# Kernel tuning notes

Hardware: AMD Instinct MI355X
Metric: run time of the kernel (lower is better)

## Reference

```python
import jax, jax.numpy as jnp
import numpy as np

N = 100000
E = 1600000
H = 4
C = 128
F_IN = 182
D = H * C  # 512
NEG_SLOPE = 0.2
LN_EPS = 1e-5


def _p(key, shape, scale=0.05):
    return jax.random.normal(key, shape, dtype=jnp.float32) * scale


def setup_inputs() -> dict:
    key = jax.random.key(0)
    ks = jax.random.split(key, 20)
    x = jax.random.normal(ks[0], (N, F_IN), dtype=jnp.float32)
    edge_index = jax.random.randint(ks[1], (2, E), 0, N, dtype=jnp.int64)
    inp = {
        "x": x,
        "edge_index": edge_index,
        # GAT layer 1
        "W1": _p(ks[2], (F_IN, D)),
        "a_src1": _p(ks[3], (H, C)),
        "a_dst1": _p(ks[4], (H, C)),
        "b1": _p(ks[5], (D,)),
        "g1": jnp.ones((D,), jnp.float32),
        "be1": jnp.zeros((D,), jnp.float32),
        # GAT layer 2
        "W2": _p(ks[6], (D, D)),
        "a_src2": _p(ks[7], (H, C)),
        "a_dst2": _p(ks[8], (H, C)),
        "b2": _p(ks[9], (D,)),
        "g2": jnp.ones((D,), jnp.float32),
        "be2": jnp.zeros((D,), jnp.float32),
        # classifier MLP
        "Wc1": _p(ks[10], (D, D)),
        "bc1": jnp.zeros((D,), jnp.float32),
        "Wc2": _p(ks[11], (D, 2)),
        "bc2": jnp.zeros((2,), jnp.float32),
    }
    return inp


def _gat_conv(x, src, dst, W, a_src, a_dst, b):
    # x: [N, Fin] -> h: [N, H, C]
    h = (x @ W).reshape(N, H, C)
    # per-node attention contributions: [N, H]
    s_src = jnp.sum(h * a_src, axis=-1)
    s_dst = jnp.sum(h * a_dst, axis=-1)
    # per-edge raw score: [E+N, H]
    e = jax.nn.leaky_relu(s_src[src] + s_dst[dst], NEG_SLOPE)
    # segment softmax over incoming edges of each dst node
    emax = jax.ops.segment_max(e, dst, num_segments=N)
    p = jnp.exp(e - emax[dst])
    denom = jax.ops.segment_sum(p, dst, num_segments=N)
    alpha = p / denom[dst]  # [E+N, H]
    # weighted aggregation of source features: [N, H, C]
    out = jax.ops.segment_sum(alpha[:, :, None] * h[src], dst, num_segments=N)
    return out.reshape(N, D) + b


def _layer_norm(x, g, b):
    mu = jnp.mean(x, axis=-1, keepdims=True)
    var = jnp.mean(jnp.square(x - mu), axis=-1, keepdims=True)
    return (x - mu) * jax.lax.rsqrt(var + LN_EPS) * g + b


def reference(x, edge_index, W1, a_src1, a_dst1, b1, g1, be1,
              W2, a_src2, a_dst2, b2, g2, be2, Wc1, bc1, Wc2, bc2):
    # add self-loops (PyG GATConv default)
    loops = jnp.arange(N, dtype=edge_index.dtype)
    src = jnp.concatenate([edge_index[0], loops])
    dst = jnp.concatenate([edge_index[1], loops])

    h1 = _gat_conv(x, src, dst, W1, a_src1, a_dst1, b1)
    h1 = jax.nn.elu(_layer_norm(h1, g1, be1))
    h2 = _gat_conv(h1, src, dst, W2, a_src2, a_dst2, b2)
    h2 = jax.nn.elu(_layer_norm(h2, g2, be2))
    # classifier (dropout is identity in eval)
    z = jax.nn.relu(h2 @ Wc1 + bc1)
    return z @ Wc2 + bc2
```

## Files before the change

### kernel.cpp

```cpp
#include <hip/hip_runtime.h>
#include <math.h>

static constexpr int N_NODES = 100000;
static constexpr int N_EDGES = 1600000;
static constexpr int E_TOT   = N_NODES + N_EDGES;
static constexpr int D   = 512;
static constexpr int FIN = 182;
static constexpr int K1P = 192;
static constexpr int M_PAD = 100096;
static constexpr float NEG_SLOPE = 0.2f;
static constexpr float LN_EPS = 1e-5f;

typedef __attribute__((ext_vector_type(8))) short short8;
typedef __attribute__((ext_vector_type(4))) float floatx4;

__device__ __forceinline__ unsigned short f2bf(float f) {
  unsigned int x = __builtin_bit_cast(unsigned int, f);
  x += 0x7fffu + ((x >> 16) & 1u);
  return (unsigned short)(x >> 16);
}
__device__ __forceinline__ void unpack2(unsigned int w, float& lo, float& hi) {
  lo = __builtin_bit_cast(float, w << 16);
  hi = __builtin_bit_cast(float, w & 0xffff0000u);
}

typedef __attribute__((address_space(1))) const void gv_t;
typedef __attribute__((address_space(3))) void lv_t;
__device__ __forceinline__ void gll16(const void* g, void* l) {
  __builtin_amdgcn_global_load_lds((gv_t*)g, (lv_t*)l, 16, 0, 0);
}

__global__ __launch_bounds__(256) void k_init(int* __restrict__ deg,
                                              int* __restrict__ counter,
                                              int* __restrict__ flag) {
  int i = blockIdx.x * 256 + threadIdx.x;
  if (i < N_NODES) deg[i] = 0;
  if (i == 0) { *counter = 0; *flag = 0; }
}

__global__ __launch_bounds__(256) void k_detect(const int* __restrict__ ei,
                                                int* __restrict__ flag) {
  bool nz = false;
#pragma unroll
  for (int r = 0; r < 8; ++r) {
    int i = threadIdx.x + r * 256;
    nz |= (ei[2 * i + 1] != 0);
  }
  __shared__ int sh[4];
  int wv = threadIdx.x >> 6;
  if ((threadIdx.x & 63) == 0) sh[wv] = 0;
  __syncthreads();
  if (__any(nz) && (threadIdx.x & 63) == 0) sh[wv] = 1;
  __syncthreads();
  if (threadIdx.x == 0) *flag = sh[0] | sh[1] | sh[2] | sh[3];
}

__device__ __forceinline__ int edge_src(const int* ei, int f, int i) {
  return f ? ei[i] : ei[2 * i];
}
__device__ __forceinline__ int edge_dst(const int* ei, int f, int i) {
  return f ? ei[N_EDGES + i] : ei[2 * (N_EDGES + i)];
}

__global__ __launch_bounds__(256) void k_count(const int* __restrict__ ei,
                                               const int* __restrict__ flag,
                                               int* __restrict__ deg) {
  int i = blockIdx.x * 256 + threadIdx.x;
  if (i >= E_TOT) return;
  int f = *flag;
  int d = (i < N_EDGES) ? edge_dst(ei, f, i) : (i - N_EDGES);
  atomicAdd(deg + d, 1);
}

__global__ __launch_bounds__(256) void k_alloc(const int* __restrict__ deg,
                                               int* __restrict__ off,
                                               int* __restrict__ pos,
                                               int* __restrict__ counter) {
  int i = blockIdx.x * 256 + threadIdx.x;
  if (i >= N_NODES) return;
  int r = atomicAdd(counter, deg[i]);
  off[i] = r;
  pos[i] = r;
}

__global__ __launch_bounds__(256) void k_fill(const int* __restrict__ ei,
                                              const int* __restrict__ flag,
                                              int* __restrict__ pos,
                                              int* __restrict__ csr_src) {
  int i = blockIdx.x * 256 + threadIdx.x;
  if (i >= E_TOT) return;
  int f = *flag;
  int s, d;
  if (i < N_EDGES) { s = edge_src(ei, f, i); d = edge_dst(ei, f, i); }
  else             { s = d = i - N_EDGES; }
  int slot = atomicAdd(pos + d, 1);
  csr_src[slot] = s;
}

__global__ __launch_bounds__(256) void k_cvt_x(const float* __restrict__ x,
                                               unsigned short* __restrict__ xb) {
  int i = blockIdx.x * 256 + threadIdx.x;
  if (i >= N_NODES * K1P) return;
  int row = i / K1P, col = i - row * K1P;
  float v = (col < FIN) ? x[(size_t)row * FIN + col] : 0.f;
  xb[i] = f2bf(v);
}

__global__ __launch_bounds__(256) void k_cvt_wt(const float* __restrict__ W,
                                                unsigned short* __restrict__ Wt,
                                                int K, int Kpad) {
  int i = blockIdx.x * 256 + threadIdx.x;
  if (i >= 512 * Kpad) return;
  int n = i / Kpad, k = i - n * Kpad;
  Wt[i] = f2bf(k < K ? W[(size_t)k * 512 + n] : 0.f);
}

__global__ __launch_bounds__(256) void k_out_init(const float* __restrict__ bc2,
                                                  float* __restrict__ out) {
  int i = blockIdx.x * 256 + threadIdx.x;
  if (i < N_NODES) {
    float2 v; v.x = bc2[0]; v.y = bc2[1];
    ((float2*)out)[i] = v;
  }
}

__global__ __launch_bounds__(256)
void gemm_mfma(const unsigned short* __restrict__ A,
               const unsigned short* __restrict__ Bt,
               unsigned short* __restrict__ C,
               int lda)
{
  __shared__ unsigned short As[128 * 32];
  __shared__ unsigned short Bs[128 * 32];
  const int t    = threadIdx.x;
  const int w    = t >> 6;
  const int lane = t & 63;
  const int r    = lane & 15;
  const int q    = lane >> 4;
  const int bm   = blockIdx.y * 128;
  const int bn   = blockIdx.x * 128;
  const int wm   = (w >> 1) * 64;
  const int wn   = (w & 1) * 64;

  const int ch0 = (w * 2 + 0) * 64 + lane;
  const int ch1 = (w * 2 + 1) * 64 + lane;
  const unsigned short* gA0 = A + (size_t)(bm + (ch0 >> 2)) * lda + (ch0 & 3) * 8;
  const unsigned short* gA1 = A + (size_t)(bm + (ch1 >> 2)) * lda + (ch1 & 3) * 8;
  const unsigned short* gB0 = Bt + (size_t)(bn + (ch0 >> 2)) * lda + (ch0 & 3) * 8;
  const unsigned short* gB1 = Bt + (size_t)(bn + (ch1 >> 2)) * lda + (ch1 & 3) * 8;
  unsigned short* lA0 = As + (w * 2 + 0) * 512;
  unsigned short* lA1 = As + (w * 2 + 1) * 512;
  unsigned short* lB0 = Bs + (w * 2 + 0) * 512;
  unsigned short* lB1 = Bs + (w * 2 + 1) * 512;

  floatx4 acc[4][4] = {};

  for (int k0 = 0; k0 < lda; k0 += 32) {
    gll16(gA0 + k0, lA0);
    gll16(gA1 + k0, lA1);
    gll16(gB0 + k0, lB0);
    gll16(gB1 + k0, lB1);
    __syncthreads();

    short8 af[4], bfr[4];
#pragma unroll
    for (int im = 0; im < 4; ++im)
      af[im] = *(const short8*)(As + (wm + im * 16 + r) * 32 + q * 8);
#pragma unroll
    for (int in = 0; in < 4; ++in)
      bfr[in] = *(const short8*)(Bs + (wn + in * 16 + r) * 32 + q * 8);
#pragma unroll
    for (int im = 0; im < 4; ++im)
#pragma unroll
      for (int in = 0; in < 4; ++in)
        acc[im][in] = __builtin_amdgcn_mfma_f32_16x16x32_bf16(
            af[im], bfr[in], acc[im][in], 0, 0, 0);
    __syncthreads();
  }

#pragma unroll
  for (int in = 0; in < 4; ++in) {
    const int col = bn + wn + in * 16 + r;
#pragma unroll
    for (int im = 0; im < 4; ++im) {
      const size_t rowbase = (size_t)(bm + wm + im * 16 + q * 4) * 512 + col;
#pragma unroll
      for (int rr = 0; rr < 4; ++rr)
        C[rowbase + (size_t)rr * 512] = f2bf(acc[im][in][rr]);
    }
  }
}

__global__ __launch_bounds__(256)
void gemm_cls(const unsigned short* __restrict__ A,
              const unsigned short* __restrict__ Bt,
              const float* __restrict__ bc1,
              const float* __restrict__ Wc2,
              float* __restrict__ out,
              int lda)
{
  __shared__ unsigned short As[128 * 32];
  __shared__ unsigned short Bs[128 * 32];
  const int t    = threadIdx.x;
  const int w    = t >> 6;
  const int lane = t & 63;
  const int r    = lane & 15;
  const int q    = lane >> 4;
  const int bm   = blockIdx.y * 128;
  const int bn   = blockIdx.x * 128;
  const int wm   = (w >> 1) * 64;
  const int wn   = (w & 1) * 64;

  const int ch0 = (w * 2 + 0) * 64 + lane;
  const int ch1 = (w * 2 + 1) * 64 + lane;
  const unsigned short* gA0 = A + (size_t)(bm + (ch0 >> 2)) * lda + (ch0 & 3) * 8;
  const unsigned short* gA1 = A + (size_t)(bm + (ch1 >> 2)) * lda + (ch1 & 3) * 8;
  const unsigned short* gB0 = Bt + (size_t)(bn + (ch0 >> 2)) * lda + (ch0 & 3) * 8;
  const unsigned short* gB1 = Bt + (size_t)(bn + (ch1 >> 2)) * lda + (ch1 & 3) * 8;
  unsigned short* lA0 = As + (w * 2 + 0) * 512;
  unsigned short* lA1 = As + (w * 2 + 1) * 512;
  unsigned short* lB0 = Bs + (w * 2 + 0) * 512;
  unsigned short* lB1 = Bs + (w * 2 + 1) * 512;

  floatx4 acc[4][4] = {};

  for (int k0 = 0; k0 < lda; k0 += 32) {
    gll16(gA0 + k0, lA0);
    gll16(gA1 + k0, lA1);
    gll16(gB0 + k0, lB0);
    gll16(gB1 + k0, lB1);
    __syncthreads();

    short8 af[4], bfr[4];
#pragma unroll
    for (int im = 0; im < 4; ++im)
      af[im] = *(const short8*)(As + (wm + im * 16 + r) * 32 + q * 8);
#pragma unroll
    for (int in = 0; in < 4; ++in)
      bfr[in] = *(const short8*)(Bs + (wn + in * 16 + r) * 32 + q * 8);
#pragma unroll
    for (int im = 0; im < 4; ++im)
#pragma unroll
      for (int in = 0; in < 4; ++in)
        acc[im][in] = __builtin_amdgcn_mfma_f32_16x16x32_bf16(
            af[im], bfr[in], acc[im][in], 0, 0, 0);
    __syncthreads();
  }

  float p0[16], p1[16];
#pragma unroll
  for (int k = 0; k < 16; ++k) { p0[k] = 0.f; p1[k] = 0.f; }

#pragma unroll
  for (int in = 0; in < 4; ++in) {
    const int col = bn + wn + in * 16 + r;
    const float bv = bc1[col];
    const float w0 = Wc2[col * 2 + 0];
    const float w1 = Wc2[col * 2 + 1];
#pragma unroll
    for (int im = 0; im < 4; ++im)
#pragma unroll
      for (int rr = 0; rr < 4; ++rr) {
        float z = fmaxf(acc[im][in][rr] + bv, 0.f);
        p0[im * 4 + rr] += z * w0;
        p1[im * 4 + rr] += z * w1;
      }
  }
#pragma unroll
  for (int o2 = 1; o2 < 16; o2 <<= 1) {
#pragma unroll
    for (int k = 0; k < 16; ++k) {
      p0[k] += __shfl_xor(p0[k], o2);
      p1[k] += __shfl_xor(p1[k], o2);
    }
  }
  if (r == 0) {
#pragma unroll
    for (int im = 0; im < 4; ++im)
#pragma unroll
      for (int rr = 0; rr < 4; ++rr) {
        int row = bm + wm + im * 16 + q * 4 + rr;
        if (row < N_NODES) {
          atomicAdd(out + (size_t)row * 2,     p0[im * 4 + rr]);
          atomicAdd(out + (size_t)row * 2 + 1, p1[im * 4 + rr]);
        }
      }
  }
}

__global__ __launch_bounds__(256) void k_sdots(const unsigned short* __restrict__ h,
                                               const float* __restrict__ a_src,
                                               const float* __restrict__ a_dst,
                                               float* __restrict__ s_src,
                                               float* __restrict__ s_dst,
                                               unsigned char* __restrict__ h8,
                                               float* __restrict__ scales) {
  int node = blockIdx.x * 4 + (threadIdx.x >> 6);
  int lane = threadIdx.x & 63;
  if (node >= N_NODES) return;
  uint4 w = ((const uint4*)(h + (size_t)node * D))[lane];
  float v[8];
  unpack2(w.x, v[0], v[1]); unpack2(w.y, v[2], v[3]);
  unpack2(w.z, v[4], v[5]); unpack2(w.w, v[6], v[7]);

  float am = 0.f;
#pragma unroll
  for (int k = 0; k < 8; ++k) am = fmaxf(am, fabsf(v[k]));
#pragma unroll
  for (int o = 1; o < 64; o <<= 1) am = fmaxf(am, __shfl_xor(am, o));
  am = fmaxf(am, 1e-20f);
  const float inv = 127.f / am;
  int qv[8];
#pragma unroll
  for (int k = 0; k < 8; ++k) qv[k] = (int)rintf(v[k] * inv);
  uint2 pk;
  pk.x = (qv[0] & 255) | ((qv[1] & 255) << 8) | ((qv[2] & 255) << 16) | ((qv[3] & 255) << 24);
  pk.y = (qv[4] & 255) | ((qv[5] & 255) << 8) | ((qv[6] & 255) << 16) | ((qv[7] & 255) << 24);
  ((uint2*)(h8 + (size_t)node * 512))[lane] = pk;
  if (lane == 0) scales[node] = am * (1.f / 127.f);

  const float4* as = (const float4*)a_src;
  const float4* ad = (const float4*)a_dst;
  float4 s0 = as[lane*2], s1 = as[lane*2+1];
  float4 d0 = ad[lane*2], d1 = ad[lane*2+1];
  float ps = v[0]*s0.x + v[1]*s0.y + v[2]*s0.z + v[3]*s0.w
           + v[4]*s1.x + v[5]*s1.y + v[6]*s1.z + v[7]*s1.w;
  float pd = v[0]*d0.x + v[1]*d0.y + v[2]*d0.z + v[3]*d0.w
           + v[4]*d1.x + v[5]*d1.y + v[6]*d1.z + v[7]*d1.w;
#pragma unroll
  for (int o = 1; o < 16; o <<= 1) {
    ps += __shfl_xor(ps, o);
    pd += __shfl_xor(pd, o);
  }
  if ((lane & 15) == 0) {
    int hh = lane >> 4;
    s_src[node*4 + hh] = ps;
    s_dst[node*4 + hh] = pd;
  }
}

__global__ __launch_bounds__(256) void k_aggregate(const unsigned char* __restrict__ h8,
                                                   const float* __restrict__ scales,
                                                   const int* __restrict__ csr_src,
                                                   const int* __restrict__ off,
                                                   const int* __restrict__ deg,
                                                   const float* __restrict__ s_src,
                                                   const float* __restrict__ s_dst,
                                                   const float* __restrict__ bvec,
                                                   const float* __restrict__ gvec,
                                                   const float* __restrict__ bevec,
                                                   unsigned short* __restrict__ out) {
  int node = blockIdx.x * 4 + (threadIdx.x >> 6);
  int lane = threadIdx.x & 63;
  if (node >= N_NODES) return;
  const int o   = __builtin_amdgcn_readfirstlane(off[node]);
  const int cnt = __builtin_amdgcn_readfirstlane(deg[node]);
  const int head = lane >> 4;
  const float sdH = s_dst[(size_t)node * 4 + head];

  float acc[8] = {0.f,0.f,0.f,0.f,0.f,0.f,0.f,0.f};
  float sum = 0.f;

  int s_cur = __builtin_amdgcn_readfirstlane(csr_src[o]);
  uint2 w_cur = ((const uint2*)(h8 + (size_t)s_cur * 512))[lane];
  float f_cur = s_src[(size_t)s_cur * 4 + head];
  float sc_cur = scales[s_cur];

  for (int j = 0; j < cnt; ++j) {
    int jn = (j + 1 < cnt) ? (j + 1) : j;
    int s_nxt = __builtin_amdgcn_readfirstlane(csr_src[o + jn]);
    uint2 w_nxt = ((const uint2*)(h8 + (size_t)s_nxt * 512))[lane];
    float f_nxt = s_src[(size_t)s_nxt * 4 + head];
    float sc_nxt = scales[s_nxt];

    float e = f_cur + sdH;
    e = (e > 0.f) ? e : NEG_SLOPE * e;
    float p = __expf(e);
    sum += p;
    float ps = p * sc_cur;
    int wx = (int)w_cur.x, wy = (int)w_cur.y;
    acc[0] += ps * (float)((wx << 24) >> 24);
    acc[1] += ps * (float)((wx << 16) >> 24);
    acc[2] += ps * (float)((wx <<  8) >> 24);
    acc[3] += ps * (float)( wx        >> 24);
    acc[4] += ps * (float)((wy << 24) >> 24);
    acc[5] += ps * (float)((wy << 16) >> 24);
    acc[6] += ps * (float)((wy <<  8) >> 24);
    acc[7] += ps * (float)( wy        >> 24);

    s_cur = s_nxt; w_cur = w_nxt; f_cur = f_nxt; sc_cur = sc_nxt;
  }

  const float inv = 1.f / sum;
  const float4* bb = (const float4*)bvec;
  float4 b0 = bb[lane*2], b1 = bb[lane*2+1];
  float bl[8] = {b0.x,b0.y,b0.z,b0.w,b1.x,b1.y,b1.z,b1.w};
#pragma unroll
  for (int k = 0; k < 8; ++k) acc[k] = acc[k] * inv + bl[k];

  float ps2 = 0.f, pq = 0.f;
#pragma unroll
  for (int k = 0; k < 8; ++k) { ps2 += acc[k]; pq += acc[k]*acc[k]; }
#pragma unroll
  for (int o2 = 1; o2 < 64; o2 <<= 1) {
    ps2 += __shfl_xor(ps2, o2);
    pq  += __shfl_xor(pq, o2);
  }
  float mu  = ps2 * (1.f/512.f);
  float var = pq * (1.f/512.f) - mu*mu;
  float rstd = rsqrtf(var + LN_EPS);

  const float4* gg = (const float4*)gvec;
  const float4* ee = (const float4*)bevec;
  float4 g0 = gg[lane*2], g1 = gg[lane*2+1];
  float4 e0 = ee[lane*2], e1 = ee[lane*2+1];
  float gs[8] = {g0.x,g0.y,g0.z,g0.w,g1.x,g1.y,g1.z,g1.w};
  float es[8] = {e0.x,e0.y,e0.z,e0.w,e1.x,e1.y,e1.z,e1.w};

  unsigned short us[8];
#pragma unroll
  for (int k = 0; k < 8; ++k) {
    float y = (acc[k] - mu) * rstd * gs[k] + es[k];
    y = (y > 0.f) ? y : expm1f(y);
    us[k] = f2bf(y);
  }
  uint4 w;
  w.x = (unsigned int)us[0] | ((unsigned int)us[1] << 16);
  w.y = (unsigned int)us[2] | ((unsigned int)us[3] << 16);
  w.z = (unsigned int)us[4] | ((unsigned int)us[5] << 16);
  w.w = (unsigned int)us[6] | ((unsigned int)us[7] << 16);
  ((uint4*)(out + (size_t)node * D))[lane] = w;
}

extern "C" void kernel_launch(void* const* d_in, const int* in_sizes, int n_in,
                              void* d_out, int out_size, void* d_ws, size_t ws_size,
                              hipStream_t stream) {
  const float* x      = (const float*)d_in[0];
  const int*   ei     = (const int*)  d_in[1];
  const float* W1     = (const float*)d_in[2];
  const float* a_src1 = (const float*)d_in[3];
  const float* a_dst1 = (const float*)d_in[4];
  const float* b1     = (const float*)d_in[5];
  const float* g1     = (const float*)d_in[6];
  const float* be1    = (const float*)d_in[7];
  const float* W2     = (const float*)d_in[8];
  const float* a_src2 = (const float*)d_in[9];
  const float* a_dst2 = (const float*)d_in[10];
  const float* b2     = (const float*)d_in[11];
  const float* g2     = (const float*)d_in[12];
  const float* be2    = (const float*)d_in[13];
  const float* Wc1    = (const float*)d_in[14];
  const float* bc1    = (const float*)d_in[15];
  const float* Wc2    = (const float*)d_in[16];
  const float* bc2    = (const float*)d_in[17];
  float* outp = (float*)d_out;

  char* p = (char*)d_ws;
  auto alloc = [&](size_t bytes) {
    char* r = p;
    p += (bytes + 255) & ~(size_t)255;
    return r;
  };
  unsigned short* hbuf = (unsigned short*)alloc((size_t)M_PAD * D * 2);
  unsigned short* obuf = (unsigned short*)alloc((size_t)M_PAD * D * 2);
  unsigned short* w1t  = (unsigned short*)alloc((size_t)512 * K1P * 2);
  unsigned short* w2t  = (unsigned short*)alloc((size_t)512 * 512 * 2);
  unsigned short* wc1t = (unsigned short*)alloc((size_t)512 * 512 * 2);
  int*   csr_src = (int*)  alloc((size_t)E_TOT * 4);
  int*   deg     = (int*)  alloc((size_t)N_NODES * 4);
  int*   off     = (int*)  alloc((size_t)N_NODES * 4);
  int*   pos     = (int*)  alloc((size_t)N_NODES * 4);
  int*   counter = (int*)  alloc(256);
  int*   flag    = (int*)  alloc(256);
  float* s_src   = (float*)alloc((size_t)N_NODES * 4 * 4);
  float* s_dst   = (float*)alloc((size_t)N_NODES * 4 * 4);
  unsigned char* h8 = (unsigned char*)alloc((size_t)M_PAD * 512);
  float* scales  = (float*)alloc((size_t)M_PAD * 4);
  unsigned short* xb = obuf;

  const int EB = (E_TOT + 255) / 256;
  const int NB = (N_NODES + 255) / 256;
  const int NW = (N_NODES + 3) / 4;
  dim3 gg(4, M_PAD / 128);

  k_init  <<<NB, 256, 0, stream>>>(deg, counter, flag);
  k_detect<<<1, 256, 0, stream>>>(ei, flag);
  k_count <<<EB, 256, 0, stream>>>(ei, flag, deg);
  k_alloc <<<NB, 256, 0, stream>>>(deg, off, pos, counter);
  k_fill  <<<EB, 256, 0, stream>>>(ei, flag, pos, csr_src);

  k_cvt_x <<<(N_NODES * K1P + 255) / 256, 256, 0, stream>>>(x, xb);
  k_cvt_wt<<<(512 * K1P + 255) / 256, 256, 0, stream>>>(W1, w1t, FIN, K1P);
  k_cvt_wt<<<(512 * 512 + 255) / 256, 256, 0, stream>>>(W2, w2t, 512, 512);
  k_cvt_wt<<<(512 * 512 + 255) / 256, 256, 0, stream>>>(Wc1, wc1t, 512, 512);
  k_out_init<<<NB, 256, 0, stream>>>(bc2, outp);

  gemm_mfma  <<<gg, 256, 0, stream>>>(xb, w1t, hbuf, K1P);
  k_sdots    <<<NW, 256, 0, stream>>>(hbuf, a_src1, a_dst1, s_src, s_dst, h8, scales);
  k_aggregate<<<NW, 256, 0, stream>>>(h8, scales, csr_src, off, deg, s_src, s_dst, b1, g1, be1, obuf);

  gemm_mfma  <<<gg, 256, 0, stream>>>(obuf, w2t, hbuf, 512);
  k_sdots    <<<NW, 256, 0, stream>>>(hbuf, a_src2, a_dst2, s_src, s_dst, h8, scales);
  k_aggregate<<<NW, 256, 0, stream>>>(h8, scales, csr_src, off, deg, s_src, s_dst, b2, g2, be2, obuf);

  gemm_cls   <<<gg, 256, 0, stream>>>(obuf, wc1t, bc1, Wc2, outp, 512);
}
```

Measured before the change: 1.023 ms.

## Fuse int8 quantization and attention dot products into GEMM epilogue

Fold the per-node int8 quantization and the s_src/s_dst attention dot products into the GEMM epilogue, so the bf16 hidden buffer is never written to or read back from memory. Quantization scales become per-head, since each block covers one 128-column head, and the aggregation kernel reads them per head. The dot products are combined with atomics into buffers that must be zeroed first. The grid is also remapped to a 1D band-grouped order so the four column tiles of a row band run close together for L2 reuse. Extra epilogue work and atomics add register pressure and cost in exchange.

```diff
diff --git a/kernel.cpp b/kernel.cpp
--- a/kernel.cpp
+++ b/kernel.cpp
@@ -8,6 +8,7 @@
 static constexpr int FIN = 182;
 static constexpr int K1P = 192;
 static constexpr int M_PAD = 100096;
+static constexpr int N_BANDS = M_PAD / 128;
 static constexpr float NEG_SLOPE = 0.2f;
 static constexpr float LN_EPS = 1e-5f;
 
@@ -124,23 +125,47 @@
   }
 }
 
+__global__ __launch_bounds__(256) void k_zero(float* __restrict__ a,
+                                              float* __restrict__ b) {
+  int i = blockIdx.x * 256 + threadIdx.x;
+  if (i < N_NODES * 4) { a[i] = 0.f; b[i] = 0.f; }
+}
+
+__device__ __forceinline__ bool band_decode(int& bm, int& bn) {
+  const int id  = blockIdx.x;
+  const int kk  = id >> 3;
+  const int band = (kk >> 2) * 8 + (id & 7);
+  if (band >= N_BANDS) return false;
+  bm = band * 128;
+  bn = (kk & 3) * 128;
+  return true;
+}
+
 __global__ __launch_bounds__(256)
-void gemm_mfma(const unsigned short* __restrict__ A,
-               const unsigned short* __restrict__ Bt,
-               unsigned short* __restrict__ C,
-               int lda)
+void gemm_fused(const unsigned short* __restrict__ A,
+                const unsigned short* __restrict__ Bt,
+                const float* __restrict__ a_src,
+                const float* __restrict__ a_dst,
+                unsigned char* __restrict__ h8,
+                float* __restrict__ scales4,
+                float* __restrict__ s_src,
+                float* __restrict__ s_dst,
+                int lda)
 {
   __shared__ unsigned short As[128 * 32];
   __shared__ unsigned short Bs[128 * 32];
+  __shared__ float sMax[2][128];
+  int bm, bn;
+  if (!band_decode(bm, bn)) return;
   const int t    = threadIdx.x;
   const int w    = t >> 6;
   const int lane = t & 63;
   const int r    = lane & 15;
   const int q    = lane >> 4;
-  const int bm   = blockIdx.y * 128;
-  const int bn   = blockIdx.x * 128;
   const int wm   = (w >> 1) * 64;
   const int wn   = (w & 1) * 64;
+  const int half = wn >> 6;
+  const int head = bn >> 7;
 
   const int ch0 = (w * 2 + 0) * 64 + lane;
   const int ch1 = (w * 2 + 1) * 64 + lane;
@@ -174,19 +199,75 @@
 #pragma unroll
       for (int in = 0; in < 4; ++in)
         acc[im][in] = __builtin_amdgcn_mfma_f32_16x16x32_bf16(
-            af[im], bfr[in], acc[im][in], 0, 0, 0);
+            bfr[in], af[im], acc[im][in], 0, 0, 0);
     __syncthreads();
   }
 
+  float am[4];
+#pragma unroll
+  for (int im = 0; im < 4; ++im) {
+    float a = 0.f;
+#pragma unroll
+    for (int in = 0; in < 4; ++in)
+#pragma unroll
+      for (int rr = 0; rr < 4; ++rr)
+        a = fmaxf(a, fabsf(acc[im][in][rr]));
+    a = fmaxf(a, __shfl_xor(a, 16));
+    a = fmaxf(a, __shfl_xor(a, 32));
+    am[im] = a;
+  }
+  if (q == 0) {
+#pragma unroll
+    for (int im = 0; im < 4; ++im) sMax[half][wm + im * 16 + r] = am[im];
+  }
+  __syncthreads();
+
+#pragma unroll
+  for (int im = 0; im < 4; ++im) {
+    const int lr = wm + im * 16 + r;
+    const int gm = bm + lr;
+    const float amv = fmaxf(fmaxf(sMax[0][lr], sMax[1][lr]), 1e-20f);
+    if (half == 0 && q == 0)
+      scales4[(size_t)gm * 4 + head] = amv * (1.f / 127.f);
+    const float qs = 127.f / amv;
+    unsigned char* hrow = h8 + (size_t)gm * 512 + bn + wn;
+#pragma unroll
+    for (int in = 0; in < 4; ++in) {
+      int q0 = (int)rintf(acc[im][in][0] * qs);
+      int q1 = (int)rintf(acc[im][in][1] * qs);
+      int q2 = (int)rintf(acc[im][in][2] * qs);
+      int q3 = (int)rintf(acc[im][in][3] * qs);
+      unsigned int pk = (q0 & 255) | ((q1 & 255) << 8) |
+                        ((q2 & 255) << 16) | ((q3 & 255) << 24);
+      *(unsigned int*)(hrow + in * 16 + q * 4) = pk;
+    }
+  }
+
+  float4 av[4], dv[4];
 #pragma unroll
   for (int in = 0; in < 4; ++in) {
-    const int col = bn + wn + in * 16 + r;
-#pragma unroll
-    for (int im = 0; im < 4; ++im) {
-      const size_t rowbase = (size_t)(bm + wm + im * 16 + q * 4) * 512 + col;
-#pragma unroll
-      for (int rr = 0; rr < 4; ++rr)
-        C[rowbase + (size_t)rr * 512] = f2bf(acc[im][in][rr]);
+    const int nb = bn + wn + in * 16 + q * 4;
+    av[in] = *(const float4*)(a_src + nb);
+    dv[in] = *(const float4*)(a_dst + nb);
+  }
+#pragma unroll
+  for (int im = 0; im < 4; ++im) {
+    float s = 0.f, d = 0.f;
+#pragma unroll
+    for (int in = 0; in < 4; ++in) {
+      s += acc[im][in][0] * av[in].x + acc[im][in][1] * av[in].y
+         + acc[im][in][2] * av[in].z + acc[im][in][3] * av[in].w;
+      d += acc[im][in][0] * dv[in].x + acc[im][in][1] * dv[in].y
+         + acc[im][in][2] * dv[in].z + acc[im][in][3] * dv[in].w;
+    }
+    s += __shfl_xor(s, 16); s += __shfl_xor(s, 32);
+    d += __shfl_xor(d, 16); d += __shfl_xor(d, 32);
+    if (q == 0) {
+      const int gm = bm + wm + im * 16 + r;
+      if (gm < N_NODES) {
+        atomicAdd(s_src + (size_t)gm * 4 + head, s);
+        atomicAdd(s_dst + (size_t)gm * 4 + head, d);
+      }
     }
   }
 }
@@ -201,13 +282,13 @@
 {
   __shared__ unsigned short As[128 * 32];
   __shared__ unsigned short Bs[128 * 32];
+  int bm, bn;
+  if (!band_decode(bm, bn)) return;
   const int t    = threadIdx.x;
   const int w    = t >> 6;
   const int lane = t & 63;
   const int r    = lane & 15;
   const int q    = lane >> 4;
-  const int bm   = blockIdx.y * 128;
-  const int bn   = blockIdx.x * 128;
   const int wm   = (w >> 1) * 64;
   const int wn   = (w & 1) * 64;
 
@@ -288,59 +369,8 @@
   }
 }
 
-__global__ __launch_bounds__(256) void k_sdots(const unsigned short* __restrict__ h,
-                                               const float* __restrict__ a_src,
-                                               const float* __restrict__ a_dst,
-                                               float* __restrict__ s_src,
-                                               float* __restrict__ s_dst,
-                                               unsigned char* __restrict__ h8,
-                                               float* __restrict__ scales) {
-  int node = blockIdx.x * 4 + (threadIdx.x >> 6);
-  int lane = threadIdx.x & 63;
-  if (node >= N_NODES) return;
-  uint4 w = ((const uint4*)(h + (size_t)node * D))[lane];
-  float v[8];
-  unpack2(w.x, v[0], v[1]); unpack2(w.y, v[2], v[3]);
-  unpack2(w.z, v[4], v[5]); unpack2(w.w, v[6], v[7]);
-
-  float am = 0.f;
-#pragma unroll
-  for (int k = 0; k < 8; ++k) am = fmaxf(am, fabsf(v[k]));
-#pragma unroll
-  for (int o = 1; o < 64; o <<= 1) am = fmaxf(am, __shfl_xor(am, o));
-  am = fmaxf(am, 1e-20f);
-  const float inv = 127.f / am;
-  int qv[8];
-#pragma unroll
-  for (int k = 0; k < 8; ++k) qv[k] = (int)rintf(v[k] * inv);
-  uint2 pk;
-  pk.x = (qv[0] & 255) | ((qv[1] & 255) << 8) | ((qv[2] & 255) << 16) | ((qv[3] & 255) << 24);
-  pk.y = (qv[4] & 255) | ((qv[5] & 255) << 8) | ((qv[6] & 255) << 16) | ((qv[7] & 255) << 24);
-  ((uint2*)(h8 + (size_t)node * 512))[lane] = pk;
-  if (lane == 0) scales[node] = am * (1.f / 127.f);
-
-  const float4* as = (const float4*)a_src;
-  const float4* ad = (const float4*)a_dst;
-  float4 s0 = as[lane*2], s1 = as[lane*2+1];
-  float4 d0 = ad[lane*2], d1 = ad[lane*2+1];
-  float ps = v[0]*s0.x + v[1]*s0.y + v[2]*s0.z + v[3]*s0.w
-           + v[4]*s1.x + v[5]*s1.y + v[6]*s1.z + v[7]*s1.w;
-  float pd = v[0]*d0.x + v[1]*d0.y + v[2]*d0.z + v[3]*d0.w
-           + v[4]*d1.x + v[5]*d1.y + v[6]*d1.z + v[7]*d1.w;
-#pragma unroll
-  for (int o = 1; o < 16; o <<= 1) {
-    ps += __shfl_xor(ps, o);
-    pd += __shfl_xor(pd, o);
-  }
-  if ((lane & 15) == 0) {
-    int hh = lane >> 4;
-    s_src[node*4 + hh] = ps;
-    s_dst[node*4 + hh] = pd;
-  }
-}
-
 __global__ __launch_bounds__(256) void k_aggregate(const unsigned char* __restrict__ h8,
-                                                   const float* __restrict__ scales,
+                                                   const float* __restrict__ scales4,
                                                    const int* __restrict__ csr_src,
                                                    const int* __restrict__ off,
                                                    const int* __restrict__ deg,
@@ -364,14 +394,14 @@
   int s_cur = __builtin_amdgcn_readfirstlane(csr_src[o]);
   uint2 w_cur = ((const uint2*)(h8 + (size_t)s_cur * 512))[lane];
   float f_cur = s_src[(size_t)s_cur * 4 + head];
-  float sc_cur = scales[s_cur];
+  float sc_cur = scales4[(size_t)s_cur * 4 + head];
 
   for (int j = 0; j < cnt; ++j) {
     int jn = (j + 1 < cnt) ? (j + 1) : j;
     int s_nxt = __builtin_amdgcn_readfirstlane(csr_src[o + jn]);
     uint2 w_nxt = ((const uint2*)(h8 + (size_t)s_nxt * 512))[lane];
     float f_nxt = s_src[(size_t)s_nxt * 4 + head];
-    float sc_nxt = scales[s_nxt];
+    float sc_nxt = scales4[(size_t)s_nxt * 4 + head];
 
     float e = f_cur + sdH;
     e = (e > 0.f) ? e : NEG_SLOPE * e;
@@ -461,8 +491,8 @@
     p += (bytes + 255) & ~(size_t)255;
     return r;
   };
-  unsigned short* hbuf = (unsigned short*)alloc((size_t)M_PAD * D * 2);
   unsigned short* obuf = (unsigned short*)alloc((size_t)M_PAD * D * 2);
+  unsigned char*  h8   = (unsigned char*)alloc((size_t)M_PAD * 512);
   unsigned short* w1t  = (unsigned short*)alloc((size_t)512 * K1P * 2);
   unsigned short* w2t  = (unsigned short*)alloc((size_t)512 * 512 * 2);
   unsigned short* wc1t = (unsigned short*)alloc((size_t)512 * 512 * 2);
@@ -474,14 +504,14 @@
   int*   flag    = (int*)  alloc(256);
   float* s_src   = (float*)alloc((size_t)N_NODES * 4 * 4);
   float* s_dst   = (float*)alloc((size_t)N_NODES * 4 * 4);
-  unsigned char* h8 = (unsigned char*)alloc((size_t)M_PAD * 512);
-  float* scales  = (float*)alloc((size_t)M_PAD * 4);
+  float* scales4 = (float*)alloc((size_t)M_PAD * 4 * 4);
   unsigned short* xb = obuf;
 
   const int EB = (E_TOT + 255) / 256;
   const int NB = (N_NODES + 255) / 256;
+  const int ZB = (N_NODES * 4 + 255) / 256;
   const int NW = (N_NODES + 3) / 4;
-  dim3 gg(4, M_PAD / 128);
+  const int GB = 8 * ((N_BANDS + 7) / 8) * 4;
 
   k_init  <<<NB, 256, 0, stream>>>(deg, counter, flag);
   k_detect<<<1, 256, 0, stream>>>(ei, flag);
@@ -495,13 +525,17 @@
   k_cvt_wt<<<(512 * 512 + 255) / 256, 256, 0, stream>>>(Wc1, wc1t, 512, 512);
   k_out_init<<<NB, 256, 0, stream>>>(bc2, outp);
 
-  gemm_mfma  <<<gg, 256, 0, stream>>>(xb, w1t, hbuf, K1P);
-  k_sdots    <<<NW, 256, 0, stream>>>(hbuf, a_src1, a_dst1, s_src, s_dst, h8, scales);
-  k_aggregate<<<NW, 256, 0, stream>>>(h8, scales, csr_src, off, deg, s_src, s_dst, b1, g1, be1, obuf);
-
-  gemm_mfma  <<<gg, 256, 0, stream>>>(obuf, w2t, hbuf, 512);
-  k_sdots    <<<NW, 256, 0, stream>>>(hbuf, a_src2, a_dst2, s_src, s_dst, h8, scales);
-  k_aggregate<<<NW, 256, 0, stream>>>(h8, scales, csr_src, off, deg, s_src, s_dst, b2, g2, be2, obuf);
-
-  gemm_cls   <<<gg, 256, 0, stream>>>(obuf, wc1t, bc1, Wc2, outp, 512);
-}
+  k_zero     <<<ZB, 256, 0, stream>>>(s_src, s_dst);
+  gemm_fused <<<GB, 256, 0, stream>>>(xb, w1t, a_src1, a_dst1, h8, scales4,
+                                      s_src, s_dst, K1P);
+  k_aggregate<<<NW, 256, 0, stream>>>(h8, scales4, csr_src, off, deg,
+                                      s_src, s_dst, b1, g1, be1, obuf);
+
+  k_zero     <<<ZB, 256, 0, stream>>>(s_src, s_dst);
+  gemm_fused <<<GB, 256, 0, stream>>>(obuf, w2t, a_src2, a_dst2, h8, scales4,
+                                      s_src, s_dst, 512);
+  k_aggregate<<<NW, 256, 0, stream>>>(h8, scales4, csr_src, off, deg,
+                                      s_src, s_dst, b2, g2, be2, obuf);
+
+  gemm_cls   <<<GB, 256, 0, stream>>>(obuf, wc1t, bc1, Wc2, outp, 512);
+}
```

New measurement: 1.037 ms. Within noise of the previous version (+1.4%).
